# Kernel tuning notes

Hardware: AMD Instinct MI355X
Metric: run time of the kernel (lower is better)

## Reference

```python
import jax, jax.numpy as jnp
import numpy as np

N_USER = 100000
N_ITEM = 100000
E = 1600000
B = 16384
D = 128
LAYERS = [128, 128]
NEG_SLOPE = 0.2
EPS = 1e-12


def _l2norm(x):
    # F.normalize(x, dim=1, p=2): x / max(||x||, eps)
    n = jnp.sqrt(jnp.sum(x * x, axis=1, keepdims=True))
    return x / jnp.maximum(n, EPS)


def _sage_layer(h, src, dst, W_self, W_neigh, b):
    # DGL SAGEConv('mean'): mean-aggregate neighbor feats, then
    # fc_self(h) + fc_neigh(h_neigh) + bias
    msg = h[src]                                   # [E, D_in] gather
    agg = jax.ops.segment_sum(msg, dst, num_segments=h.shape[0])
    deg = jax.ops.segment_sum(jnp.ones((src.shape[0],), h.dtype), dst,
                              num_segments=h.shape[0])
    h_neigh = agg / jnp.maximum(deg, 1.0)[:, None]  # zero in-degree -> 0
    out = h @ W_self + h_neigh @ W_neigh + b
    return jax.nn.leaky_relu(out, NEG_SLOPE)


def setup_inputs() -> dict:
    key = jax.random.key(0)
    ks = jax.random.split(key, 20)
    inp = {}
    inp["src"] = jax.random.randint(ks[0], (E,), 0, N_USER)
    inp["dst"] = jax.random.randint(ks[1], (E,), 0, N_USER)
    inp["users"] = jax.random.randint(ks[2], (B,), 0, N_USER)
    inp["pos_items"] = jax.random.randint(ks[3], (B,), 0, N_ITEM)
    inp["neg_items"] = jax.random.randint(ks[4], (B,), 0, N_ITEM)
    inp["user_feat"] = jax.random.normal(ks[5], (N_USER, D), jnp.float32) * 0.05
    inp["item_feat"] = jax.random.normal(ks[6], (N_ITEM, D), jnp.float32) * 0.05
    dims = [D] + LAYERS
    i = 7
    for l in range(len(LAYERS)):
        di, do = dims[l], dims[l + 1]
        s = 1.0 / np.sqrt(di)
        inp[f"Wu_self{l}"] = jax.random.normal(ks[i], (di, do), jnp.float32) * s; i += 1
        inp[f"Wu_neigh{l}"] = jax.random.normal(ks[i], (di, do), jnp.float32) * s; i += 1
        inp[f"bu{l}"] = jnp.zeros((do,), jnp.float32)
        inp[f"Wi{l}"] = jax.random.normal(ks[i], (di, do), jnp.float32) * s; i += 1
        inp[f"bi{l}"] = jnp.zeros((do,), jnp.float32)
    return inp


def reference(src, dst, users, pos_items, neg_items, user_feat, item_feat,
              Wu_self0, Wu_neigh0, bu0, Wi0, bi0,
              Wu_self1, Wu_neigh1, bu1, Wi1, bi1):
    user_params = [(Wu_self0, Wu_neigh0, bu0), (Wu_self1, Wu_neigh1, bu1)]
    item_params = [(Wi0, bi0), (Wi1, bi1)]

    h_u = user_feat
    user_embeds = [h_u]
    for (Ws, Wn, b) in user_params:
        h_u = _sage_layer(h_u, src, dst, Ws, Wn, b)
        h_u = _l2norm(h_u)  # dropout p=0 -> identity
        user_embeds.append(h_u)

    h_i = item_feat
    item_embeds = [h_i]
    for (W, b) in item_params:
        h_i = jax.nn.leaky_relu(h_i @ W + b, NEG_SLOPE)
        h_i = _l2norm(h_i)
        item_embeds.append(h_i)

    user_embd = jnp.concatenate(user_embeds, axis=1)   # [N_user, 3*D]
    item_embd = jnp.concatenate(item_embeds, axis=1)   # [N_item, 3*D]

    return (user_embd[users], item_embd[pos_items], item_embd[neg_items])
```

## Files before the change

### kernel.cpp

```cpp
#include <hip/hip_runtime.h>

#define NU 100000
#define NI 100000
#define NE 1600000
#define BB 16384
#define DD 128

static constexpr int SCAN_CHUNK = 2048;
static constexpr int SCAN_NBLK  = (NU + SCAN_CHUNK - 1) / SCAN_CHUNK;
static constexpr int USER_TILES = NU / 16;

static constexpr int NXCD   = 8;
static constexpr int DRANGE = NU / NXCD;
static constexpr int K_CH   = 32;
static constexpr int CHUNK4 = NE / 4 / K_CH;
static constexpr int HIST_BLKS = NXCD * K_CH;
static constexpr int PACK_BLKS = 48;
static constexpr int CVT_UNIT  = 2048;
static constexpr int CVT_TOT   = NU * 32;
static constexpr int CVT_BLKS  = (CVT_TOT + CVT_UNIT - 1) / CVT_UNIT;

static constexpr size_t OFF_DEG      = 0;
static constexpr size_t OFF_ROWSTART = 400128;
static constexpr size_t OFF_BSUM     = 1200384;
static constexpr size_t OFF_EDGESRC  = 1200640;
static constexpr size_t OFF_H1       = 7600640;
static constexpr size_t OFF_WFRAG    = 58800640;


typedef __bf16 bf16x8 __attribute__((ext_vector_type(8)));
typedef float f32x4 __attribute__((ext_vector_type(4)));
typedef unsigned int u32x4 __attribute__((ext_vector_type(4)));

union frag_u {
    u32x4 u;
    bf16x8 b;
    unsigned short us[8];
};

__device__ __forceinline__ unsigned short f2bf(float f) {
    unsigned u = __float_as_uint(f);
    u = (u + 0x7fffu + ((u >> 16) & 1u)) >> 16;
    return (unsigned short)u;
}

__device__ __forceinline__ unsigned pack_bf16_pair(float a, float b) {
    return (unsigned)f2bf(a) | ((unsigned)f2bf(b) << 16);
}

__device__ __forceinline__ float2 unpack_bf16_pair(unsigned u) {
    float2 r;
    r.x = __uint_as_float(u << 16);
    r.y = __uint_as_float(u & 0xffff0000u);
    return r;
}

__device__ __forceinline__ f32x4 mfma16(bf16x8 a, bf16x8 b, f32x4 c) {
    return __builtin_amdgcn_mfma_f32_16x16x32_bf16(a, b, c, 0, 0, 0);
}

__device__ __forceinline__ bf16x8 bfrag(const u32x4* __restrict__ wf, int idx) {
    frag_u f;
    f.u = wf[idx];
    return f.b;
}

__device__ __forceinline__ void make_afrag_hilo(const float* rowp, int kb,
                                                bf16x8* hi, bf16x8* lo) {
    float4 v0 = *(const float4*)(rowp + kb);
    float4 v1 = *(const float4*)(rowp + kb + 4);
    float vv[8] = {v0.x, v0.y, v0.z, v0.w, v1.x, v1.y, v1.z, v1.w};
    frag_u h, l;
    #pragma unroll
    for (int e = 0; e < 8; ++e) {
        unsigned short hb = f2bf(vv[e]);
        h.us[e] = hb;
        float hf = __uint_as_float(((unsigned)hb) << 16);
        l.us[e] = f2bf(vv[e] - hf);
    }
    *hi = h.b;
    *lo = l.b;
}

__global__ __launch_bounds__(256) void mega_prep(
    const int* __restrict__ dst, int* __restrict__ hist,
    const float* __restrict__ uf, unsigned* __restrict__ ubf,
    const float* __restrict__ Ws0, const float* __restrict__ Wn0,
    const float* __restrict__ Ws1, const float* __restrict__ Wn1,
    const float* __restrict__ Wi0, const float* __restrict__ Wi1,
    u32x4* __restrict__ wfrag) {
    __shared__ int h[DRANGE];
    int t = threadIdx.x;
    if (blockIdx.x < HIST_BLKS) {
        int r = blockIdx.x & (NXCD - 1);
        int k = blockIdx.x >> 3;
        for (int j = t; j < DRANGE; j += 256) h[j] = 0;
        __syncthreads();
        int lo = r * DRANGE;
        const int4* d4 = (const int4*)dst + (size_t)k * CHUNK4;
        for (int i = t; i < CHUNK4; i += 256) {
            int4 d = d4[i];
            if ((unsigned)(d.x - lo) < (unsigned)DRANGE) atomicAdd(&h[d.x - lo], 1);
            if ((unsigned)(d.y - lo) < (unsigned)DRANGE) atomicAdd(&h[d.y - lo], 1);
            if ((unsigned)(d.z - lo) < (unsigned)DRANGE) atomicAdd(&h[d.z - lo], 1);
            if ((unsigned)(d.w - lo) < (unsigned)DRANGE) atomicAdd(&h[d.w - lo], 1);
        }
        __syncthreads();
        int* hb = hist + (size_t)(r * K_CH + k) * DRANGE;
        for (int j = t; j < DRANGE; j += 256) hb[j] = h[j];
    } else if (blockIdx.x < HIST_BLKS + PACK_BLKS) {
        int i = (blockIdx.x - HIST_BLKS) * 256 + t;
        const float* tab[6] = {Ws0, Wn0, Ws1, Wn1, Wi0, Wi1};
        int matg = i >> 11;
        int j = (i >> 8) & 7, kk = (i >> 6) & 3, ln = i & 63;
        const float* W = tab[matg];
        int n = j * 16 + (ln & 15);
        int kb = kk * 32 + (ln >> 4) * 8;
        unsigned short u[8];
        #pragma unroll
        for (int e = 0; e < 8; ++e) u[e] = f2bf(W[(size_t)(kb + e) * DD + n]);
        u32x4 w;
        w[0] = u[0] | ((unsigned)u[1] << 16);
        w[1] = u[2] | ((unsigned)u[3] << 16);
        w[2] = u[4] | ((unsigned)u[5] << 16);
        w[3] = u[6] | ((unsigned)u[7] << 16);
        wfrag[i] = w;
    } else {
        int bid2 = blockIdx.x - HIST_BLKS - PACK_BLKS;
        const float4* uf4 = (const float4*)uf;
        uint2* ub2 = (uint2*)ubf;
        #pragma unroll
        for (int it = 0; it < 8; ++it) {
            int idx = bid2 * CVT_UNIT + it * 256 + t;
            if (idx < CVT_TOT) {
                float4 v = uf4[idx];
                uint2 o;
                o.x = pack_bf16_pair(v.x, v.y);
                o.y = pack_bf16_pair(v.z, v.w);
                ub2[idx] = o;
            }
        }
    }
}

__global__ __launch_bounds__(256) void deg_reduce(const int* __restrict__ hist,
                                                  int* __restrict__ deg) {
    int d = blockIdx.x * 256 + threadIdx.x;
    if (d >= NU) return;
    int r = d / DRANGE, j = d - r * DRANGE;
    const int* hb = hist + (size_t)r * K_CH * DRANGE + j;
    int s = 0;
    #pragma unroll
    for (int k = 0; k < K_CH; ++k) s += hb[(size_t)k * DRANGE];
    deg[d] = s;
}

__global__ __launch_bounds__(256) void scan1_kernel(const int* __restrict__ deg,
                                                    int* __restrict__ bsum) {
    __shared__ int sh[256];
    int t = threadIdx.x;
    int base = blockIdx.x * SCAN_CHUNK + t * 8;
    int s = 0;
    #pragma unroll
    for (int j = 0; j < 8; ++j) {
        int idx = base + j;
        s += (idx < NU) ? deg[idx] : 0;
    }
    sh[t] = s;
    __syncthreads();
    for (int off = 128; off > 0; off >>= 1) {
        if (t < off) sh[t] += sh[t + off];
        __syncthreads();
    }
    if (t == 0) bsum[blockIdx.x] = sh[0];
}

__global__ void scan2_kernel(int* __restrict__ bsum) {
    if (threadIdx.x == 0) {
        int acc = 0;
        for (int i = 0; i < SCAN_NBLK; ++i) {
            int v = bsum[i];
            bsum[i] = acc;
            acc += v;
        }
    }
}

__global__ __launch_bounds__(256) void scan3_kernel(const int* __restrict__ deg,
                                                    const int* __restrict__ bsum,
                                                    int* __restrict__ row_start) {
    __shared__ int sh[256];
    int t = threadIdx.x;
    int base = blockIdx.x * SCAN_CHUNK + t * 8;
    int v[8];
    int s = 0;
    #pragma unroll
    for (int j = 0; j < 8; ++j) {
        int idx = base + j;
        v[j] = (idx < NU) ? deg[idx] : 0;
        s += v[j];
    }
    sh[t] = s;
    __syncthreads();
    for (int off = 1; off < 256; off <<= 1) {
        int val = sh[t];
        int add = (t >= off) ? sh[t - off] : 0;
        __syncthreads();
        sh[t] = val + add;
        __syncthreads();
    }
    int excl = sh[t] - s + bsum[blockIdx.x];
    #pragma unroll
    for (int j = 0; j < 8; ++j) {
        int idx = base + j;
        if (idx < NU) row_start[idx] = excl;
        excl += v[j];
    }
}

__global__ __launch_bounds__(256) void base_kernel(const int* __restrict__ row_start,
                                                   int* __restrict__ hist) {
    int d = blockIdx.x * 256 + threadIdx.x;
    if (d >= NU) return;
    int r = d / DRANGE, j = d - r * DRANGE;
    int* hb = hist + (size_t)r * K_CH * DRANGE + j;
    int acc = row_start[d];
    #pragma unroll
    for (int k = 0; k < K_CH; ++k) {
        int c = hb[(size_t)k * DRANGE];
        hb[(size_t)k * DRANGE] = acc;
        acc += c;
    }
}

__global__ __launch_bounds__(256) void fill2(const int* __restrict__ src,
                                             const int* __restrict__ dst,
                                             const int* __restrict__ base,
                                             int* __restrict__ edge_src) {
    __shared__ int cur[DRANGE];
    int r = blockIdx.x & (NXCD - 1);
    int k = blockIdx.x >> 3;
    int t = threadIdx.x;
    const int* bb = base + (size_t)(r * K_CH + k) * DRANGE;
    for (int j = t; j < DRANGE; j += 256) cur[j] = bb[j];
    __syncthreads();
    int lo = r * DRANGE;
    const int4* d4 = (const int4*)dst + (size_t)k * CHUNK4;
    const int4* s4 = (const int4*)src + (size_t)k * CHUNK4;
    for (int i = t; i < CHUNK4; i += 256) {
        int4 d = d4[i];
        int4 s = s4[i];
        if ((unsigned)(d.x - lo) < (unsigned)DRANGE) edge_src[atomicAdd(&cur[d.x - lo], 1)] = s.x;
        if ((unsigned)(d.y - lo) < (unsigned)DRANGE) edge_src[atomicAdd(&cur[d.y - lo], 1)] = s.y;
        if ((unsigned)(d.z - lo) < (unsigned)DRANGE) edge_src[atomicAdd(&cur[d.z - lo], 1)] = s.z;
        if ((unsigned)(d.w - lo) < (unsigned)DRANGE) edge_src[atomicAdd(&cur[d.w - lo], 1)] = s.w;
    }
}

__global__ __launch_bounds__(256) void agg_kernel(const unsigned* __restrict__ ubf,
                                                  const int* __restrict__ row_start,
                                                  const int* __restrict__ deg,
                                                  const int* __restrict__ edge_src,
                                                  unsigned* __restrict__ hn) {
    int wid = blockIdx.x * 4 + (threadIdx.x >> 6);
    int lane = threadIdx.x & 63;
    if (wid >= NU) return;
    int st = row_start[wid];
    int dg = deg[wid];
    int lanelet = lane & 15;
    int eslot = lane >> 4;
    float acc[8] = {0.f, 0.f, 0.f, 0.f, 0.f, 0.f, 0.f, 0.f};
    const unsigned* colp = ubf + (lanelet << 2);
    for (int base = 0; base < dg; base += 64) {
        int n = min(dg - base, 64);
        int myidx = (lane < n) ? edge_src[st + base + lane] : 0;
        int e = 0;
        #pragma unroll 2
        for (; e + 4 <= n; e += 4) {
            int s = __shfl(myidx, e + eslot, 64);
            u32x4 v = *(const u32x4*)(colp + (size_t)s * 64);
            #pragma unroll
            for (int k = 0; k < 4; ++k) {
                float2 f = unpack_bf16_pair(v[k]);
                acc[2 * k] += f.x;
                acc[2 * k + 1] += f.y;
            }
        }
        int rem = n - e;
        int s = __shfl(myidx, min(e + eslot, 63), 64);
        if (eslot < rem) {
            u32x4 v = *(const u32x4*)(colp + (size_t)s * 64);
            #pragma unroll
            for (int k = 0; k < 4; ++k) {
                float2 f = unpack_bf16_pair(v[k]);
                acc[2 * k] += f.x;
                acc[2 * k + 1] += f.y;
            }
        }
    }
    #pragma unroll
    for (int k = 0; k < 8; ++k) {
        acc[k] += __shfl_xor(acc[k], 16, 64);
        acc[k] += __shfl_xor(acc[k], 32, 64);
    }
    float inv = 1.0f / fmaxf((float)dg, 1.0f);
    if (eslot == 0) {
        u32x4 o;
        o[0] = pack_bf16_pair(acc[0] * inv, acc[1] * inv);
        o[1] = pack_bf16_pair(acc[2] * inv, acc[3] * inv);
        o[2] = pack_bf16_pair(acc[4] * inv, acc[5] * inv);
        o[3] = pack_bf16_pair(acc[6] * inv, acc[7] * inv);
        *(u32x4*)(hn + (size_t)wid * 64 + (lanelet << 2)) = o;
    }
}

__global__ __launch_bounds__(256) void user_mm_mfma(
    const float* __restrict__ hself, const unsigned short* __restrict__ hn,
    const u32x4* __restrict__ wf, const float* __restrict__ bias,
    float* __restrict__ out) {
    int t = threadIdx.x;
    int lane = t & 63;
    int tile = blockIdx.x * 4 + (t >> 6);
    if (tile >= USER_TILES) return;
    int gbase = tile * 16;
    int m = lane & 15, q = lane >> 4;
    const float* selfp = hself + (size_t)(gbase + m) * DD;
    const unsigned short* neighp = hn + (size_t)(gbase + m) * DD;
    bf16x8 as_hi[4], as_lo[4], an[4];
    #pragma unroll
    for (int kk = 0; kk < 4; ++kk) {
        int kb = kk * 32 + q * 8;
        make_afrag_hilo(selfp, kb, &as_hi[kk], &as_lo[kk]);
        frag_u f;
        f.u = *(const u32x4*)(neighp + kb);
        an[kk] = f.b;
    }
    f32x4 acc[8];
    f32x4 zero = {0.f, 0.f, 0.f, 0.f};
    #pragma unroll
    for (int j = 0; j < 8; ++j) acc[j] = zero;
    #pragma unroll 2
    for (int j = 0; j < 8; ++j) {
        #pragma unroll
        for (int kk = 0; kk < 4; ++kk) {
            bf16x8 bs = bfrag(wf, (j * 4 + kk) * 64 + lane);
            acc[j] = mfma16(as_hi[kk], bs, acc[j]);
            acc[j] = mfma16(as_lo[kk], bs, acc[j]);
            bf16x8 bn = bfrag(wf, 2048 + (j * 4 + kk) * 64 + lane);
            acc[j] = mfma16(an[kk], bn, acc[j]);
        }
    }
    float ss[4] = {0.f, 0.f, 0.f, 0.f};
    #pragma unroll
    for (int j = 0; j < 8; ++j) {
        float bj = bias[j * 16 + m];
        #pragma unroll
        for (int r = 0; r < 4; ++r) {
            float x = acc[j][r] + bj;
            x = x > 0.f ? x : 0.2f * x;
            acc[j][r] = x;
            ss[r] += x * x;
        }
    }
    #pragma unroll
    for (int r = 0; r < 4; ++r) {
        float s = ss[r];
        s += __shfl_xor(s, 1, 64);
        s += __shfl_xor(s, 2, 64);
        s += __shfl_xor(s, 4, 64);
        s += __shfl_xor(s, 8, 64);
        ss[r] = 1.0f / fmaxf(sqrtf(s), 1e-12f);
    }
    #pragma unroll
    for (int j = 0; j < 8; ++j)
        #pragma unroll
        for (int r = 0; r < 4; ++r)
            out[(size_t)(gbase + q * 4 + r) * DD + j * 16 + m] = acc[j][r] * ss[r];
}

__global__ __launch_bounds__(256) void tail_fuse(
    const float* __restrict__ ufeat, const float* __restrict__ h1,
    const int* __restrict__ users, const int* __restrict__ row_start,
    const int* __restrict__ deg, const int* __restrict__ edge_src,
    const float* __restrict__ ifeat, const int* __restrict__ pos,
    const int* __restrict__ neg, const u32x4* __restrict__ wf_u,
    const u32x4* __restrict__ wf_i, const float* __restrict__ bu1,
    const float* __restrict__ bi0, const float* __restrict__ bi1,
    float* __restrict__ out) {
    __shared__ float sc[16 * 132];
    __shared__ float ssp[16 * 4];
    int t = threadIdx.x;
    int lane = t & 63, wave = t >> 6;
    int m = lane & 15, q = lane >> 4;
    f32x4 zero = {0.f, 0.f, 0.f, 0.f};

    if (blockIdx.x < 1024) {
        int gb = blockIdx.x * 16;
        int L = lane & 31;
        int eslot = lane >> 5;
        const float* hl = h1 + 4 * L;
        #pragma unroll
        for (int rr = 0; rr < 4; ++rr) {
            int r = wave * 4 + rr;
            int u = users[gb + r];
            int st = row_start[u], dg = deg[u];
            float ax = 0.f, ay = 0.f, az = 0.f, aw = 0.f;
            for (int base = 0; base < dg; base += 64) {
                int n = min(dg - base, 64);
                int myidx = (lane < n) ? edge_src[st + base + lane] : 0;
                int e = 0;
                #pragma unroll 4
                for (; e + 2 <= n; e += 2) {
                    int s = __shfl(myidx, e + eslot, 64);
                    float4 v = *(const float4*)(hl + (size_t)s * DD);
                    ax += v.x; ay += v.y; az += v.z; aw += v.w;
                }
                if (e < n) {
                    int s = __shfl(myidx, e, 64);
                    if (eslot == 0) {
                        float4 v = *(const float4*)(hl + (size_t)s * DD);
                        ax += v.x; ay += v.y; az += v.z; aw += v.w;
                    }
                }
            }
            ax += __shfl_xor(ax, 32, 64);
            ay += __shfl_xor(ay, 32, 64);
            az += __shfl_xor(az, 32, 64);
            aw += __shfl_xor(aw, 32, 64);
            float inv = 1.0f / fmaxf((float)dg, 1.0f);
            if (eslot == 0) {
                float4 o = {ax * inv, ay * inv, az * inv, aw * inv};
                *(float4*)(sc + r * 132 + 4 * L) = o;
            }
            float* orow = out + (size_t)(gb + r) * 384;
            ((float2*)orow)[lane] = ((const float2*)(ufeat + (size_t)u * DD))[lane];
            ((float2*)orow)[64 + lane] = ((const float2*)(h1 + (size_t)u * DD))[lane];
        }
        __syncthreads();
        int j0 = wave * 2;
        int um = users[gb + m];
        const float* selfp = h1 + (size_t)um * DD;
        bf16x8 sh[4], sl[4], nh[4], nl[4];
        #pragma unroll
        for (int kk = 0; kk < 4; ++kk) {
            int kb = kk * 32 + q * 8;
            make_afrag_hilo(selfp, kb, &sh[kk], &sl[kk]);
            make_afrag_hilo(sc + m * 132, kb, &nh[kk], &nl[kk]);
        }
        f32x4 a0 = zero, a1 = zero;
        #pragma unroll
        for (int kk = 0; kk < 4; ++kk) {
            bf16x8 b0 = bfrag(wf_u, (j0 * 4 + kk) * 64 + lane);
            a0 = mfma16(sh[kk], b0, a0);
            a0 = mfma16(sl[kk], b0, a0);
            bf16x8 n0 = bfrag(wf_u, 2048 + (j0 * 4 + kk) * 64 + lane);
            a0 = mfma16(nh[kk], n0, a0);
            a0 = mfma16(nl[kk], n0, a0);
            bf16x8 b1 = bfrag(wf_u, ((j0 + 1) * 4 + kk) * 64 + lane);
            a1 = mfma16(sh[kk], b1, a1);
            a1 = mfma16(sl[kk], b1, a1);
            bf16x8 n1 = bfrag(wf_u, 2048 + ((j0 + 1) * 4 + kk) * 64 + lane);
            a1 = mfma16(nh[kk], n1, a1);
            a1 = mfma16(nl[kk], n1, a1);
        }
        float bj0 = bu1[j0 * 16 + m], bj1 = bu1[(j0 + 1) * 16 + m];
        float ss[4];
        #pragma unroll
        for (int r = 0; r < 4; ++r) {
            float x0 = a0[r] + bj0; x0 = x0 > 0.f ? x0 : 0.2f * x0; a0[r] = x0;
            float x1 = a1[r] + bj1; x1 = x1 > 0.f ? x1 : 0.2f * x1; a1[r] = x1;
            float s = x0 * x0 + x1 * x1;
            s += __shfl_xor(s, 1, 64);
            s += __shfl_xor(s, 2, 64);
            s += __shfl_xor(s, 4, 64);
            s += __shfl_xor(s, 8, 64);
            ss[r] = s;
        }
        if (m == 0) {
            #pragma unroll
            for (int r = 0; r < 4; ++r) ssp[(q * 4 + r) * 4 + wave] = ss[r];
        }
        __syncthreads();
        #pragma unroll
        for (int r = 0; r < 4; ++r) {
            int row = q * 4 + r;
            float tot = ssp[row * 4] + ssp[row * 4 + 1] + ssp[row * 4 + 2] + ssp[row * 4 + 3];
            float inv = 1.0f / fmaxf(sqrtf(tot), 1e-12f);
            out[(size_t)(gb + row) * 384 + 256 + j0 * 16 + m] = a0[r] * inv;
            out[(size_t)(gb + row) * 384 + 256 + (j0 + 1) * 16 + m] = a1[r] * inv;
        }
        return;
    }

    int tile = blockIdx.x - 1024;
    int gb = tile * 16;
    int j0 = wave * 2;
    int rowm = gb + m;
    int idxm = (rowm < BB) ? pos[rowm] : neg[rowm - BB];
    const float* rowp = ifeat + (size_t)idxm * DD;
    bf16x8 ahi[4], alo[4];
    #pragma unroll
    for (int kk = 0; kk < 4; ++kk)
        make_afrag_hilo(rowp, kk * 32 + q * 8, &ahi[kk], &alo[kk]);
    f32x4 a0 = zero, a1 = zero;
    #pragma unroll
    for (int kk = 0; kk < 4; ++kk) {
        bf16x8 b0 = bfrag(wf_i, (j0 * 4 + kk) * 64 + lane);
        a0 = mfma16(ahi[kk], b0, a0);
        a0 = mfma16(alo[kk], b0, a0);
        bf16x8 b1 = bfrag(wf_i, ((j0 + 1) * 4 + kk) * 64 + lane);
        a1 = mfma16(ahi[kk], b1, a1);
        a1 = mfma16(alo[kk], b1, a1);
    }
    {
        float bj0 = bi0[j0 * 16 + m], bj1 = bi0[(j0 + 1) * 16 + m];
        float ss[4];
        #pragma unroll
        for (int r = 0; r < 4; ++r) {
            float x0 = a0[r] + bj0; x0 = x0 > 0.f ? x0 : 0.2f * x0; a0[r] = x0;
            float x1 = a1[r] + bj1; x1 = x1 > 0.f ? x1 : 0.2f * x1; a1[r] = x1;
            float s = x0 * x0 + x1 * x1;
            s += __shfl_xor(s, 1, 64);
            s += __shfl_xor(s, 2, 64);
            s += __shfl_xor(s, 4, 64);
            s += __shfl_xor(s, 8, 64);
            ss[r] = s;
        }
        if (m == 0) {
            #pragma unroll
            for (int r = 0; r < 4; ++r) ssp[(q * 4 + r) * 4 + wave] = ss[r];
        }
        __syncthreads();
        #pragma unroll
        for (int r = 0; r < 4; ++r) {
            int row = q * 4 + r;
            float tot = ssp[row * 4] + ssp[row * 4 + 1] + ssp[row * 4 + 2] + ssp[row * 4 + 3];
            float inv = 1.0f / fmaxf(sqrtf(tot), 1e-12f);
            sc[row * 132 + j0 * 16 + m] = a0[r] * inv;
            sc[row * 132 + (j0 + 1) * 16 + m] = a1[r] * inv;
        }
        __syncthreads();
    }
    #pragma unroll
    for (int rr = 0; rr < 4; ++rr) {
        int r = wave * 4 + rr;
        int row = gb + r;
        int idx = (row < BB) ? pos[row] : neg[row - BB];
        float* orow = out + (size_t)(BB + row) * 384;
        ((float2*)orow)[lane] = ((const float2*)(ifeat + (size_t)idx * DD))[lane];
        float2 r1v;
        r1v.x = sc[r * 132 + 2 * lane];
        r1v.y = sc[r * 132 + 2 * lane + 1];
        ((float2*)orow)[64 + lane] = r1v;
    }
    bf16x8 chi[4], clo[4];
    #pragma unroll
    for (int kk = 0; kk < 4; ++kk)
        make_afrag_hilo(sc + m * 132, kk * 32 + q * 8, &chi[kk], &clo[kk]);
    a0 = zero; a1 = zero;
    #pragma unroll
    for (int kk = 0; kk < 4; ++kk) {
        bf16x8 b0 = bfrag(wf_i, 2048 + (j0 * 4 + kk) * 64 + lane);
        a0 = mfma16(chi[kk], b0, a0);
        a0 = mfma16(clo[kk], b0, a0);
        bf16x8 b1 = bfrag(wf_i, 2048 + ((j0 + 1) * 4 + kk) * 64 + lane);
        a1 = mfma16(chi[kk], b1, a1);
        a1 = mfma16(clo[kk], b1, a1);
    }
    {
        float bj0 = bi1[j0 * 16 + m], bj1 = bi1[(j0 + 1) * 16 + m];
        float ss[4];
        #pragma unroll
        for (int r = 0; r < 4; ++r) {
            float x0 = a0[r] + bj0; x0 = x0 > 0.f ? x0 : 0.2f * x0; a0[r] = x0;
            float x1 = a1[r] + bj1; x1 = x1 > 0.f ? x1 : 0.2f * x1; a1[r] = x1;
            float s = x0 * x0 + x1 * x1;
            s += __shfl_xor(s, 1, 64);
            s += __shfl_xor(s, 2, 64);
            s += __shfl_xor(s, 4, 64);
            s += __shfl_xor(s, 8, 64);
            ss[r] = s;
        }
        __syncthreads();
        if (m == 0) {
            #pragma unroll
            for (int r = 0; r < 4; ++r) ssp[(q * 4 + r) * 4 + wave] = ss[r];
        }
        __syncthreads();
        #pragma unroll
        for (int r = 0; r < 4; ++r) {
            int row = q * 4 + r;
            float tot = ssp[row * 4] + ssp[row * 4 + 1] + ssp[row * 4 + 2] + ssp[row * 4 + 3];
            float inv = 1.0f / fmaxf(sqrtf(tot), 1e-12f);
            out[(size_t)(BB + gb + row) * 384 + 256 + j0 * 16 + m] = a0[r] * inv;
            out[(size_t)(BB + gb + row) * 384 + 256 + (j0 + 1) * 16 + m] = a1[r] * inv;
        }
    }
}

extern "C" void kernel_launch(void* const* d_in, const int* in_sizes, int n_in,
                              void* d_out, int out_size, void* d_ws, size_t ws_size,
                              hipStream_t stream) {
    const int* src = (const int*)d_in[0];
    const int* dst = (const int*)d_in[1];
    const int* users = (const int*)d_in[2];
    const int* pos = (const int*)d_in[3];
    const int* neg = (const int*)d_in[4];
    const float* ufeat = (const float*)d_in[5];
    const float* ifeat = (const float*)d_in[6];
    const float* Ws0 = (const float*)d_in[7];
    const float* Wn0 = (const float*)d_in[8];
    const float* bu0 = (const float*)d_in[9];
    const float* Wi0 = (const float*)d_in[10];
    const float* bi0 = (const float*)d_in[11];
    const float* Ws1 = (const float*)d_in[12];
    const float* Wn1 = (const float*)d_in[13];
    const float* bu1 = (const float*)d_in[14];
    const float* Wi1 = (const float*)d_in[15];
    const float* bi1 = (const float*)d_in[16];
    float* out = (float*)d_out;

    char* ws = (char*)d_ws;
    int* deg = (int*)(ws + OFF_DEG);
    int* row_start = (int*)(ws + OFF_ROWSTART);
    int* bsum = (int*)(ws + OFF_BSUM);
    int* edge_src = (int*)(ws + OFF_EDGESRC);
    float* h1 = (float*)(ws + OFF_H1);
    u32x4* wfrag = (u32x4*)(ws + OFF_WFRAG);

    unsigned* ubf = (unsigned*)d_out;
    unsigned* hn = (unsigned*)((char*)d_out + (size_t)NU * DD * 2);
    int* hist = (int*)((char*)d_out + (size_t)NU * DD * 4);
    const unsigned short* hn_us = (const unsigned short*)hn;

    mega_prep<<<HIST_BLKS + PACK_BLKS + CVT_BLKS, 256, 0, stream>>>(
        dst, hist, ufeat, ubf, Ws0, Wn0, Ws1, Wn1, Wi0, Wi1, wfrag);
    deg_reduce<<<(NU + 255) / 256, 256, 0, stream>>>(hist, deg);
    scan1_kernel<<<SCAN_NBLK, 256, 0, stream>>>(deg, bsum);
    scan2_kernel<<<1, 64, 0, stream>>>(bsum);
    scan3_kernel<<<SCAN_NBLK, 256, 0, stream>>>(deg, bsum, row_start);
    base_kernel<<<(NU + 255) / 256, 256, 0, stream>>>(row_start, hist);
    fill2<<<HIST_BLKS, 256, 0, stream>>>(src, dst, hist, edge_src);
    agg_kernel<<<(NU + 3) / 4, 256, 0, stream>>>(ubf, row_start, deg, edge_src, hn);
    user_mm_mfma<<<(USER_TILES + 3) / 4, 256, 0, stream>>>(ufeat, hn_us, wfrag, bu0, h1);
    tail_fuse<<<1024 + 2048, 256, 0, stream>>>(ufeat, h1, users, row_start, deg, edge_src,
                                               ifeat, pos, neg, wfrag + 4096, wfrag + 8192,
                                               bu1, bi0, bi1, out);
}
```

Measured before the change: 440.1 us.

## Fuse degree reduce into scan, base into scan3, and aggregation into layer-1 MFMA

Folds the per-node histogram degree reduction into scan1 and the per-chunk base offset computation into scan3, removing two launches. It also merges neighbor mean aggregation with the layer-1 matmul: each block aggregates 16 rows into shared memory, then its four waves each compute two output column tiles with an L2 norm reduced across waves through shared memory. This drops the bf16 hn round trip through global memory but changes the aggregation parallelism (each wave handles 4 rows serially) and the scan kernels now do strided hist reads with lower parallelism.

Result: slower. 503.1 us (+14.3%).

```diff
diff --git a/kernel.cpp b/kernel.cpp
--- a/kernel.cpp
+++ b/kernel.cpp
@@ -143,19 +143,8 @@
     }
 }
 
-__global__ __launch_bounds__(256) void deg_reduce(const int* __restrict__ hist,
-                                                  int* __restrict__ deg) {
-    int d = blockIdx.x * 256 + threadIdx.x;
-    if (d >= NU) return;
-    int r = d / DRANGE, j = d - r * DRANGE;
-    const int* hb = hist + (size_t)r * K_CH * DRANGE + j;
-    int s = 0;
-    #pragma unroll
-    for (int k = 0; k < K_CH; ++k) s += hb[(size_t)k * DRANGE];
-    deg[d] = s;
-}
-
-__global__ __launch_bounds__(256) void scan1_kernel(const int* __restrict__ deg,
+__global__ __launch_bounds__(256) void scan1_kernel(const int* __restrict__ hist,
+                                                    int* __restrict__ deg,
                                                     int* __restrict__ bsum) {
     __shared__ int sh[256];
     int t = threadIdx.x;
@@ -164,7 +153,15 @@
     #pragma unroll
     for (int j = 0; j < 8; ++j) {
         int idx = base + j;
-        s += (idx < NU) ? deg[idx] : 0;
+        if (idx < NU) {
+            int r = idx / DRANGE, jj = idx - r * DRANGE;
+            const int* hb = hist + (size_t)r * K_CH * DRANGE + jj;
+            int d = 0;
+            #pragma unroll
+            for (int k = 0; k < K_CH; ++k) d += hb[(size_t)k * DRANGE];
+            deg[idx] = d;
+            s += d;
+        }
     }
     sh[t] = s;
     __syncthreads();
@@ -188,7 +185,8 @@
 
 __global__ __launch_bounds__(256) void scan3_kernel(const int* __restrict__ deg,
                                                     const int* __restrict__ bsum,
-                                                    int* __restrict__ row_start) {
+                                                    int* __restrict__ row_start,
+                                                    int* __restrict__ hist) {
     __shared__ int sh[256];
     int t = threadIdx.x;
     int base = blockIdx.x * SCAN_CHUNK + t * 8;
@@ -213,23 +211,19 @@
     #pragma unroll
     for (int j = 0; j < 8; ++j) {
         int idx = base + j;
-        if (idx < NU) row_start[idx] = excl;
+        if (idx < NU) {
+            row_start[idx] = excl;
+            int r = idx / DRANGE, jj = idx - r * DRANGE;
+            int* hb = hist + (size_t)r * K_CH * DRANGE + jj;
+            int acc = excl;
+            #pragma unroll
+            for (int k = 0; k < K_CH; ++k) {
+                int c = hb[(size_t)k * DRANGE];
+                hb[(size_t)k * DRANGE] = acc;
+                acc += c;
+            }
+        }
         excl += v[j];
-    }
-}
-
-__global__ __launch_bounds__(256) void base_kernel(const int* __restrict__ row_start,
-                                                   int* __restrict__ hist) {
-    int d = blockIdx.x * 256 + threadIdx.x;
-    if (d >= NU) return;
-    int r = d / DRANGE, j = d - r * DRANGE;
-    int* hb = hist + (size_t)r * K_CH * DRANGE + j;
-    int acc = row_start[d];
-    #pragma unroll
-    for (int k = 0; k < K_CH; ++k) {
-        int c = hb[(size_t)k * DRANGE];
-        hb[(size_t)k * DRANGE] = acc;
-        acc += c;
     }
 }
 
@@ -257,125 +251,121 @@
     }
 }
 
-__global__ __launch_bounds__(256) void agg_kernel(const unsigned* __restrict__ ubf,
-                                                  const int* __restrict__ row_start,
-                                                  const int* __restrict__ deg,
-                                                  const int* __restrict__ edge_src,
-                                                  unsigned* __restrict__ hn) {
-    int wid = blockIdx.x * 4 + (threadIdx.x >> 6);
-    int lane = threadIdx.x & 63;
-    if (wid >= NU) return;
-    int st = row_start[wid];
-    int dg = deg[wid];
+__global__ __launch_bounds__(256) void l1_fuse(
+    const unsigned* __restrict__ ubf, const float* __restrict__ ufeat,
+    const int* __restrict__ row_start, const int* __restrict__ deg,
+    const int* __restrict__ edge_src, const u32x4* __restrict__ wf,
+    const float* __restrict__ bias, float* __restrict__ h1) {
+    __shared__ float sc[16 * 132];
+    __shared__ float ssp[16 * 4];
+    int t = threadIdx.x;
+    int lane = t & 63, wave = t >> 6;
+    int gb = blockIdx.x * 16;
     int lanelet = lane & 15;
     int eslot = lane >> 4;
-    float acc[8] = {0.f, 0.f, 0.f, 0.f, 0.f, 0.f, 0.f, 0.f};
     const unsigned* colp = ubf + (lanelet << 2);
-    for (int base = 0; base < dg; base += 64) {
-        int n = min(dg - base, 64);
-        int myidx = (lane < n) ? edge_src[st + base + lane] : 0;
-        int e = 0;
-        #pragma unroll 2
-        for (; e + 4 <= n; e += 4) {
-            int s = __shfl(myidx, e + eslot, 64);
-            u32x4 v = *(const u32x4*)(colp + (size_t)s * 64);
-            #pragma unroll
-            for (int k = 0; k < 4; ++k) {
-                float2 f = unpack_bf16_pair(v[k]);
-                acc[2 * k] += f.x;
-                acc[2 * k + 1] += f.y;
+    #pragma unroll
+    for (int rr = 0; rr < 4; ++rr) {
+        int r = wave * 4 + rr;
+        int g = gb + r;
+        int st = row_start[g], dg = deg[g];
+        float acc[8] = {0.f, 0.f, 0.f, 0.f, 0.f, 0.f, 0.f, 0.f};
+        for (int base = 0; base < dg; base += 64) {
+            int n = min(dg - base, 64);
+            int myidx = (lane < n) ? edge_src[st + base + lane] : 0;
+            int e = 0;
+            #pragma unroll 2
+            for (; e + 4 <= n; e += 4) {
+                int s = __shfl(myidx, e + eslot, 64);
+                u32x4 v = *(const u32x4*)(colp + (size_t)s * 64);
+                #pragma unroll
+                for (int k = 0; k < 4; ++k) {
+                    float2 f = unpack_bf16_pair(v[k]);
+                    acc[2 * k] += f.x;
+                    acc[2 * k + 1] += f.y;
+                }
             }
-        }
-        int rem = n - e;
-        int s = __shfl(myidx, min(e + eslot, 63), 64);
-        if (eslot < rem) {
-            u32x4 v = *(const u32x4*)(colp + (size_t)s * 64);
-            #pragma unroll
-            for (int k = 0; k < 4; ++k) {
-                float2 f = unpack_bf16_pair(v[k]);
-                acc[2 * k] += f.x;
-                acc[2 * k + 1] += f.y;
+            int rem = n - e;
+            int s = __shfl(myidx, min(e + eslot, 63), 64);
+            if (eslot < rem) {
+                u32x4 v = *(const u32x4*)(colp + (size_t)s * 64);
+                #pragma unroll
+                for (int k = 0; k < 4; ++k) {
+                    float2 f = unpack_bf16_pair(v[k]);
+                    acc[2 * k] += f.x;
+                    acc[2 * k + 1] += f.y;
+                }
             }
         }
-    }
-    #pragma unroll
-    for (int k = 0; k < 8; ++k) {
-        acc[k] += __shfl_xor(acc[k], 16, 64);
-        acc[k] += __shfl_xor(acc[k], 32, 64);
-    }
-    float inv = 1.0f / fmaxf((float)dg, 1.0f);
-    if (eslot == 0) {
-        u32x4 o;
-        o[0] = pack_bf16_pair(acc[0] * inv, acc[1] * inv);
-        o[1] = pack_bf16_pair(acc[2] * inv, acc[3] * inv);
-        o[2] = pack_bf16_pair(acc[4] * inv, acc[5] * inv);
-        o[3] = pack_bf16_pair(acc[6] * inv, acc[7] * inv);
-        *(u32x4*)(hn + (size_t)wid * 64 + (lanelet << 2)) = o;
-    }
-}
-
-__global__ __launch_bounds__(256) void user_mm_mfma(
-    const float* __restrict__ hself, const unsigned short* __restrict__ hn,
-    const u32x4* __restrict__ wf, const float* __restrict__ bias,
-    float* __restrict__ out) {
-    int t = threadIdx.x;
-    int lane = t & 63;
-    int tile = blockIdx.x * 4 + (t >> 6);
-    if (tile >= USER_TILES) return;
-    int gbase = tile * 16;
+        #pragma unroll
+        for (int k = 0; k < 8; ++k) {
+            acc[k] += __shfl_xor(acc[k], 16, 64);
+            acc[k] += __shfl_xor(acc[k], 32, 64);
+        }
+        float inv = 1.0f / fmaxf((float)dg, 1.0f);
+        if (eslot == 0) {
+            float4 o0 = {acc[0] * inv, acc[1] * inv, acc[2] * inv, acc[3] * inv};
+            float4 o1 = {acc[4] * inv, acc[5] * inv, acc[6] * inv, acc[7] * inv};
+            *(float4*)(sc + r * 132 + (lanelet << 3)) = o0;
+            *(float4*)(sc + r * 132 + (lanelet << 3) + 4) = o1;
+        }
+    }
+    __syncthreads();
     int m = lane & 15, q = lane >> 4;
-    const float* selfp = hself + (size_t)(gbase + m) * DD;
-    const unsigned short* neighp = hn + (size_t)(gbase + m) * DD;
-    bf16x8 as_hi[4], as_lo[4], an[4];
+    int j0 = wave * 2;
+    const float* selfp = ufeat + (size_t)(gb + m) * DD;
+    bf16x8 sh_[4], sl_[4], nb[4];
     #pragma unroll
     for (int kk = 0; kk < 4; ++kk) {
         int kb = kk * 32 + q * 8;
-        make_afrag_hilo(selfp, kb, &as_hi[kk], &as_lo[kk]);
-        frag_u f;
-        f.u = *(const u32x4*)(neighp + kb);
-        an[kk] = f.b;
-    }
-    f32x4 acc[8];
+        make_afrag_hilo(selfp, kb, &sh_[kk], &sl_[kk]);
+        const float* np = sc + m * 132 + kb;
+        frag_u nf;
+        #pragma unroll
+        for (int e = 0; e < 8; ++e) nf.us[e] = f2bf(np[e]);
+        nb[kk] = nf.b;
+    }
     f32x4 zero = {0.f, 0.f, 0.f, 0.f};
-    #pragma unroll
-    for (int j = 0; j < 8; ++j) acc[j] = zero;
-    #pragma unroll 2
-    for (int j = 0; j < 8; ++j) {
-        #pragma unroll
-        for (int kk = 0; kk < 4; ++kk) {
-            bf16x8 bs = bfrag(wf, (j * 4 + kk) * 64 + lane);
-            acc[j] = mfma16(as_hi[kk], bs, acc[j]);
-            acc[j] = mfma16(as_lo[kk], bs, acc[j]);
-            bf16x8 bn = bfrag(wf, 2048 + (j * 4 + kk) * 64 + lane);
-            acc[j] = mfma16(an[kk], bn, acc[j]);
-        }
-    }
-    float ss[4] = {0.f, 0.f, 0.f, 0.f};
-    #pragma unroll
-    for (int j = 0; j < 8; ++j) {
-        float bj = bias[j * 16 + m];
-        #pragma unroll
-        for (int r = 0; r < 4; ++r) {
-            float x = acc[j][r] + bj;
-            x = x > 0.f ? x : 0.2f * x;
-            acc[j][r] = x;
-            ss[r] += x * x;
-        }
-    }
+    f32x4 a0 = zero, a1 = zero;
+    #pragma unroll
+    for (int kk = 0; kk < 4; ++kk) {
+        bf16x8 b0 = bfrag(wf, (j0 * 4 + kk) * 64 + lane);
+        a0 = mfma16(sh_[kk], b0, a0);
+        a0 = mfma16(sl_[kk], b0, a0);
+        bf16x8 n0 = bfrag(wf, 2048 + (j0 * 4 + kk) * 64 + lane);
+        a0 = mfma16(nb[kk], n0, a0);
+        bf16x8 b1 = bfrag(wf, ((j0 + 1) * 4 + kk) * 64 + lane);
+        a1 = mfma16(sh_[kk], b1, a1);
+        a1 = mfma16(sl_[kk], b1, a1);
+        bf16x8 n1 = bfrag(wf, 2048 + ((j0 + 1) * 4 + kk) * 64 + lane);
+        a1 = mfma16(nb[kk], n1, a1);
+    }
+    float bj0 = bias[j0 * 16 + m], bj1 = bias[(j0 + 1) * 16 + m];
+    float ss[4];
     #pragma unroll
     for (int r = 0; r < 4; ++r) {
-        float s = ss[r];
+        float x0 = a0[r] + bj0; x0 = x0 > 0.f ? x0 : 0.2f * x0; a0[r] = x0;
+        float x1 = a1[r] + bj1; x1 = x1 > 0.f ? x1 : 0.2f * x1; a1[r] = x1;
+        float s = x0 * x0 + x1 * x1;
         s += __shfl_xor(s, 1, 64);
         s += __shfl_xor(s, 2, 64);
         s += __shfl_xor(s, 4, 64);
         s += __shfl_xor(s, 8, 64);
-        ss[r] = 1.0f / fmaxf(sqrtf(s), 1e-12f);
-    }
-    #pragma unroll
-    for (int j = 0; j < 8; ++j)
-        #pragma unroll
-        for (int r = 0; r < 4; ++r)
-            out[(size_t)(gbase + q * 4 + r) * DD + j * 16 + m] = acc[j][r] * ss[r];
+        ss[r] = s;
+    }
+    if (m == 0) {
+        #pragma unroll
+        for (int r = 0; r < 4; ++r) ssp[(q * 4 + r) * 4 + wave] = ss[r];
+    }
+    __syncthreads();
+    #pragma unroll
+    for (int r = 0; r < 4; ++r) {
+        int row = q * 4 + r;
+        float tot = ssp[row * 4] + ssp[row * 4 + 1] + ssp[row * 4 + 2] + ssp[row * 4 + 3];
+        float inv = 1.0f / fmaxf(sqrtf(tot), 1e-12f);
+        h1[(size_t)(gb + row) * DD + j0 * 16 + m] = a0[r] * inv;
+        h1[(size_t)(gb + row) * DD + (j0 + 1) * 16 + m] = a1[r] * inv;
+    }
 }
 
 __global__ __launch_bounds__(256) void tail_fuse(
@@ -629,20 +619,16 @@
     u32x4* wfrag = (u32x4*)(ws + OFF_WFRAG);
 
     unsigned* ubf = (unsigned*)d_out;
-    unsigned* hn = (unsigned*)((char*)d_out + (size_t)NU * DD * 2);
     int* hist = (int*)((char*)d_out + (size_t)NU * DD * 4);
-    const unsigned short* hn_us = (const unsigned short*)hn;
 
     mega_prep<<<HIST_BLKS + PACK_BLKS + CVT_BLKS, 256, 0, stream>>>(
         dst, hist, ufeat, ubf, Ws0, Wn0, Ws1, Wn1, Wi0, Wi1, wfrag);
-    deg_reduce<<<(NU + 255) / 256, 256, 0, stream>>>(hist, deg);
-    scan1_kernel<<<SCAN_NBLK, 256, 0, stream>>>(deg, bsum);
+    scan1_kernel<<<SCAN_NBLK, 256, 0, stream>>>(hist, deg, bsum);
     scan2_kernel<<<1, 64, 0, stream>>>(bsum);
-    scan3_kernel<<<SCAN_NBLK, 256, 0, stream>>>(deg, bsum, row_start);
-    base_kernel<<<(NU + 255) / 256, 256, 0, stream>>>(row_start, hist);
+    scan3_kernel<<<SCAN_NBLK, 256, 0, stream>>>(deg, bsum, row_start, hist);
     fill2<<<HIST_BLKS, 256, 0, stream>>>(src, dst, hist, edge_src);
-    agg_kernel<<<(NU + 3) / 4, 256, 0, stream>>>(ubf, row_start, deg, edge_src, hn);
-    user_mm_mfma<<<(USER_TILES + 3) / 4, 256, 0, stream>>>(ufeat, hn_us, wfrag, bu0, h1);
+    l1_fuse<<<USER_TILES, 256, 0, stream>>>(ubf, ufeat, row_start, deg, edge_src,
+                                            wfrag, bu0, h1);
     tail_fuse<<<1024 + 2048, 256, 0, stream>>>(ufeat, h1, users, row_start, deg, edge_src,
                                                ifeat, pos, neg, wfrag + 4096, wfrag + 8192,
                                                bu1, bi0, bi1, out);
```
